# Optimization experiments

Measured on AMD Instinct MI355X. Metric: run time of the kernel, lower is better.

Reference implementation:

```python
import jax, jax.numpy as jnp
import numpy as np

B, N, C = 8, 2048, 256

def setup_inputs() -> dict:
    key = jax.random.key(0)
    ks = jax.random.split(key, 6)
    corr = jax.random.normal(ks[0], (B, N, N), dtype=jnp.float32)
    feat = jax.random.normal(ks[1], (B, N, C), dtype=jnp.float32)
    histogram = jax.random.uniform(ks[2], (B, N, 1), dtype=jnp.float32)
    mask = jax.random.normal(ks[3], (N, N), dtype=jnp.float32)
    # nn.Linear(C, C) params
    lim = 1.0 / np.sqrt(C)
    v_w = jax.random.uniform(ks[4], (C, C), minval=-lim, maxval=lim, dtype=jnp.float32)
    v_b = jax.random.uniform(ks[5], (C,), minval=-lim, maxval=lim, dtype=jnp.float32)
    return {"corr": corr, "feat": feat, "histogram": histogram, "mask": mask, "v_w": v_w, "v_b": v_b}

def reference(corr, feat, histogram, mask, v_w, v_b):
    # histogram is viewed/expanded in the original but never used downstream.
    # masked softmax over last axis: (b, n, n)
    attn = jax.nn.softmax(corr + mask[None, :, :], axis=-1)
    # v projection: y = feat @ v_w.T + v_b   (b, n, c)
    ref_feat_v = jnp.einsum("bnc,dc->bnd", feat, v_w) + v_b
    # attention output: (b, n, c)
    return jnp.einsum("bnm,bmc->bnc", attn, ref_feat_v)
```

## Files before the change

kernel.cpp:

```cpp
#include <hip/hip_runtime.h>
#include <hip/hip_fp16.h>


#define B_ 8
#define N_ 2048
#define C_ 256

typedef _Float16 half8  __attribute__((ext_vector_type(8)));
typedef _Float16 half4v __attribute__((ext_vector_type(4)));
typedef float    f32x4  __attribute__((ext_vector_type(4)));

__global__ __launch_bounds__(256) void k_convw(const float* __restrict__ w,
                                               _Float16* __restrict__ wh) {
    int i = (blockIdx.x * 256 + threadIdx.x) * 4;
    float4 v = *(const float4*)(w + i);
    half4v h = {(_Float16)v.x, (_Float16)v.y, (_Float16)v.z, (_Float16)v.w};
    *(half4v*)(wh + i) = h;
}

__global__ __launch_bounds__(256) void k_trans(const float* __restrict__ feat,
                                               _Float16* __restrict__ featF) {
    __shared__ _Float16 s[64][68];
    int blk  = blockIdx.x;
    int b    = blk >> 7;
    int tile = blk & 127;
    int n0   = (tile >> 2) << 6;
    int c0   = (tile & 3) << 6;
    int t    = threadIdx.x;

    const float* src = feat + ((size_t)(b * N_ + n0)) * C_ + c0;
#pragma unroll
    for (int i = 0; i < 4; ++i) {
        int idx = i * 256 + t;
        int row = idx >> 4;
        int c4  = (idx & 15) << 2;
        float4 v = *(const float4*)(src + (size_t)row * C_ + c4);
        half4v h = {(_Float16)v.x, (_Float16)v.y, (_Float16)v.z, (_Float16)v.w};
        *(half4v*)&s[row][c4] = h;
    }
    __syncthreads();

    int w = t >> 6, l = t & 63;
    int kk  = w & 1;
    int cb0 = (w >> 1) << 1;
#pragma unroll
    for (int cbi = 0; cbi < 2; ++cbi) {
        int cb = cb0 + cbi;
        half8 v;
#pragma unroll
        for (int j = 0; j < 8; ++j)
            v[j] = s[kk * 32 + ((l >> 4) << 3) + j][(cb << 4) + (l & 15)];
        _Float16* dst = featF +
            (((size_t)((b * 64 + (n0 >> 5) + kk) * 16 + (c0 >> 4) + cb)) * 64 + l) * 8;
        *(half8*)dst = v;
    }
}

__global__ __launch_bounds__(512, 4) void k_attn(const float* __restrict__ corr,
                                                 const float* __restrict__ mask,
                                                 const _Float16* __restrict__ featF,
                                                 _Float16* __restrict__ T) {
    __shared__ _Float16 p_lds[2][32 * 64];
    __shared__ float rowsum[32];

    const int rblk = blockIdx.x >> 3;
    const int b    = blockIdx.x & 7;
    const int r0   = rblk * 32;
    const int tg   = threadIdx.x;
    const int w    = tg >> 6, l = tg & 63;
    const int lrow = l & 15, kch = l >> 4;

    const int srow = tg >> 4;
    const int scol = (tg & 15) << 2;

    const float*    pc  = corr + ((size_t)(b * N_ + r0 + srow)) * N_ + scol;
    const float*    pm  = mask + ((size_t)(r0 + srow)) * N_ + scol;
    const _Float16* pfb = featF + ((size_t)b * (64 * 16 * 512))
                               + (((size_t)(w * 2)) * 64 + l) * 8;

    const int swaddr = srow * 64 + (((scol >> 3) ^ (srow & 7)) << 3) + (scol & 7);
    const int ag0 = ((kch ^ (lrow & 7)) << 3);
    const int ag1 = (((4 + kch) ^ (lrow & 7)) << 3);

    float rs = 0.0f;
    f32x4 acc[2][2] = {};

#define EXPSTORE(TT, CC, MM)                                                  \
    {                                                                         \
        float p0 = __expf((CC).x + (MM).x), p1 = __expf((CC).y + (MM).y);     \
        float p2 = __expf((CC).z + (MM).z), p3 = __expf((CC).w + (MM).w);     \
        rs += (p0 + p1) + (p2 + p3);                                          \
        half4v h = {(_Float16)p0, (_Float16)p1, (_Float16)p2, (_Float16)p3};  \
        *(half4v*)&p_lds[(TT) & 1][swaddr] = h;                               \
    }

    float4 cP = *(const float4*)pc;
    float4 mP = *(const float4*)pm;
    float4 cA = *(const float4*)(pc + 64);
    float4 mA = *(const float4*)(pm + 64);
    float4 cB, mB;
    EXPSTORE(0, cP, mP);
    __syncthreads();

#define STEP(T_, CCON, MCON, CLD, MLD)                                        \
    {                                                                         \
        const int t_ = (T_);                                                  \
          \
        const _Float16* pf = pfb + (size_t)t_ * 16384;                        \
        half8 b00 = *(const half8*)pf;                                        \
        half8 b01 = *(const half8*)(pf + 512);                                \
        half8 b10 = *(const half8*)(pf + 8192);                               \
        half8 b11 = *(const half8*)(pf + 8704);                               \
                                           \
        if (t_ < 30) {                                                        \
            CLD = *(const float4*)(pc + (t_ + 2) * 64);                       \
            MLD = *(const float4*)(pm + (t_ + 2) * 64);                       \
        }                                                                     \
                                                      \
        const _Float16* pl = &p_lds[t_ & 1][0];                               \
        half8 a00 = *(const half8*)&pl[lrow * 64 + ag0];                      \
        half8 a10 = *(const half8*)&pl[(16 + lrow) * 64 + ag0];               \
        half8 a01 = *(const half8*)&pl[lrow * 64 + ag1];                      \
        half8 a11 = *(const half8*)&pl[(16 + lrow) * 64 + ag1];               \
                             \
        if (t_ < 31) EXPSTORE(t_ + 1, CCON, MCON);                            \
                        \
        acc[0][0] = __builtin_amdgcn_mfma_f32_16x16x32_f16(a00, b00, acc[0][0], 0, 0, 0); \
        acc[0][1] = __builtin_amdgcn_mfma_f32_16x16x32_f16(a00, b01, acc[0][1], 0, 0, 0); \
        acc[1][0] = __builtin_amdgcn_mfma_f32_16x16x32_f16(a10, b00, acc[1][0], 0, 0, 0); \
        acc[1][1] = __builtin_amdgcn_mfma_f32_16x16x32_f16(a10, b01, acc[1][1], 0, 0, 0); \
        acc[0][0] = __builtin_amdgcn_mfma_f32_16x16x32_f16(a01, b10, acc[0][0], 0, 0, 0); \
        acc[0][1] = __builtin_amdgcn_mfma_f32_16x16x32_f16(a01, b11, acc[0][1], 0, 0, 0); \
        acc[1][0] = __builtin_amdgcn_mfma_f32_16x16x32_f16(a11, b10, acc[1][0], 0, 0, 0); \
        acc[1][1] = __builtin_amdgcn_mfma_f32_16x16x32_f16(a11, b11, acc[1][1], 0, 0, 0); \
            \
        asm volatile("s_waitcnt lgkmcnt(0)" ::: "memory");                    \
        __builtin_amdgcn_sched_barrier(0);                                    \
        __builtin_amdgcn_s_barrier();                                         \
        __builtin_amdgcn_sched_barrier(0);                                    \
    }

    for (int th = 0; th < 16; ++th) {
        STEP(2 * th,     cA, mA, cB, mB);
        STEP(2 * th + 1, cB, mB, cA, mA);
    }
#undef STEP
#undef EXPSTORE

    rs += __shfl_xor(rs, 1);
    rs += __shfl_xor(rs, 2);
    rs += __shfl_xor(rs, 4);
    rs += __shfl_xor(rs, 8);
    if ((l & 15) == 0) rowsum[srow] = rs;
    __syncthreads();

#pragma unroll
    for (int m = 0; m < 2; ++m) {
        float inv[4];
#pragma unroll
        for (int j = 0; j < 4; ++j)
            inv[j] = 1.0f / rowsum[m * 16 + kch * 4 + j];
        _Float16* pT = T + ((size_t)(b * N_ + r0 + m * 16 + kch * 4)) * C_
                         + w * 32 + lrow;
#pragma unroll
        for (int j = 0; j < 4; ++j) {
#pragma unroll
            for (int n = 0; n < 2; ++n) {
                pT[(size_t)j * C_ + n * 16] = (_Float16)(acc[m][n][j] * inv[j]);
            }
        }
    }
}

__global__ __launch_bounds__(256, 2) void k_out(const _Float16* __restrict__ T,
                                                const _Float16* __restrict__ wh,
                                                const float* __restrict__ v_b,
                                                float* __restrict__ out) {
    const int blk = blockIdx.x;
    const int r0  = blk * 32;
    const int t   = threadIdx.x;
    const int w   = t >> 6, l = t & 63;
    const int wr  = w >> 1, wc = w & 1;
    const int lrow = l & 15, kch = l >> 4;

    const _Float16* pA = T  + ((size_t)(r0 + wr * 16 + lrow)) * C_ + kch * 8;
    const _Float16* pB = wh + ((size_t)(wc * 128 + lrow)) * C_ + kch * 8;

    f32x4 acc[8] = {};
#pragma unroll
    for (int step = 0; step < 8; step++) {
        half8 a = *(const half8*)(pA + step * 32);
#pragma unroll
        for (int q = 0; q < 8; q++) {
            half8 bf = *(const half8*)(pB + step * 32 + (size_t)q * 16 * C_);
            acc[q] = __builtin_amdgcn_mfma_f32_16x16x32_f16(a, bf, acc[q], 0, 0, 0);
        }
    }

    float* pO = out + ((size_t)(r0 + wr * 16 + kch * 4)) * C_ + wc * 128 + lrow;
#pragma unroll
    for (int q = 0; q < 8; q++) {
        float bias = v_b[wc * 128 + q * 16 + lrow];
#pragma unroll
        for (int j = 0; j < 4; j++) {
            pO[(size_t)j * C_ + q * 16] = acc[q][j] + bias;
        }
    }
}

extern "C" void kernel_launch(void* const* d_in, const int* in_sizes, int n_in,
                              void* d_out, int out_size, void* d_ws, size_t ws_size,
                              hipStream_t stream) {
    const float* corr = (const float*)d_in[0];
    const float* feat = (const float*)d_in[1];
    const float* mask = (const float*)d_in[3];
    const float* v_w  = (const float*)d_in[4];
    const float* v_b  = (const float*)d_in[5];
    float* out = (float*)d_out;

    char* ws = (char*)d_ws;
    _Float16* featF = (_Float16*)ws;
    _Float16* T     = (_Float16*)(ws + (size_t)8 * 1024 * 1024);
    _Float16* wh    = (_Float16*)(ws + (size_t)16 * 1024 * 1024);

    hipLaunchKernelGGL(k_trans, dim3(1024), dim3(256), 0, stream, feat, featF);
    hipLaunchKernelGGL(k_convw, dim3(64),   dim3(256), 0, stream, v_w, wh);
    hipLaunchKernelGGL(k_attn,  dim3(512),  dim3(512), 0, stream, corr, mask, featF, T);
    hipLaunchKernelGGL(k_out,   dim3(512),  dim3(256), 0, stream, T, wh, v_b, out);
}
```

Baseline: 75.82 us.

## Retile attention kernel to 128-row by 64-column blocks with LDS-staged features

The attention kernel now gives each block 128 rows and a 64-column slice of C, laid out as a 4x2 grid of waves. Feature tiles are staged into LDS with direct global-to-LDS loads, double-buffered, so more rows reuse each feature tile. The cost is that each row's softmax exponentials and its corr/mask reads are repeated across the four column-slice blocks. Wait counts are changed so the asynchronous loads overlap with the MFMA work.

```diff
diff --git a/kernel.cpp b/kernel.cpp
--- a/kernel.cpp
+++ b/kernel.cpp
@@ -9,6 +9,13 @@
 typedef _Float16 half8  __attribute__((ext_vector_type(8)));
 typedef _Float16 half4v __attribute__((ext_vector_type(4)));
 typedef float    f32x4  __attribute__((ext_vector_type(4)));
+
+static __device__ __forceinline__ void gload_lds16(const _Float16* g, _Float16* l) {
+    __builtin_amdgcn_global_load_lds(
+        (const __attribute__((address_space(1))) unsigned int*)g,
+        (__attribute__((address_space(3))) unsigned int*)l,
+        16, 0, 0);
+}
 
 __global__ __launch_bounds__(256) void k_convw(const float* __restrict__ w,
                                                _Float16* __restrict__ wh) {
@@ -60,71 +67,105 @@
                                                  const float* __restrict__ mask,
                                                  const _Float16* __restrict__ featF,
                                                  _Float16* __restrict__ T) {
-    __shared__ _Float16 p_lds[2][32 * 64];
-    __shared__ float rowsum[32];
-
-    const int rblk = blockIdx.x >> 3;
-    const int b    = blockIdx.x & 7;
-    const int r0   = rblk * 32;
-    const int tg   = threadIdx.x;
-    const int w    = tg >> 6, l = tg & 63;
+    __shared__ _Float16 p_lds[2][128 * 64];
+    __shared__ _Float16 f_lds[2][8 * 512];
+    __shared__ float rowsum[128];
+
+    const int blk = blockIdx.x;
+    const int b   = blk & 7;
+    const int s   = blk >> 3;
+    const int rb  = s >> 2, cb = s & 3;
+    const int r0  = rb * 128;
+    const int tg  = threadIdx.x;
+    const int w   = tg >> 6, l = tg & 63;
+    const int wr  = w >> 1, wc = w & 1;
     const int lrow = l & 15, kch = l >> 4;
 
-    const int srow = tg >> 4;
-    const int scol = (tg & 15) << 2;
-
-    const float*    pc  = corr + ((size_t)(b * N_ + r0 + srow)) * N_ + scol;
-    const float*    pm  = mask + ((size_t)(r0 + srow)) * N_ + scol;
-    const _Float16* pfb = featF + ((size_t)b * (64 * 16 * 512))
-                               + (((size_t)(w * 2)) * 64 + l) * 8;
-
-    const int swaddr = srow * 64 + (((scol >> 3) ^ (srow & 7)) << 3) + (scol & 7);
+    const int srow = tg >> 2;
+    const int scol = (tg & 3) << 4;
+
+    const float* pc = corr + ((size_t)(b * N_ + r0 + srow)) * N_ + scol;
+    const float* pm = mask + ((size_t)(r0 + srow)) * N_ + scol;
+    const _Float16* pf = featF +
+        (((size_t)(b * 64 + (w >> 2)) * 16 + cb * 4 + (w & 3)) * 512) + l * 8;
+    const int fstep = 2 * 16 * 512;
+    _Float16* fd0 = &f_lds[0][w * 512 + l * 8];
+    _Float16* fd1 = &f_lds[1][w * 512 + l * 8];
+
+    int wad[4];
+#pragma unroll
+    for (int q = 0; q < 4; ++q) {
+        int col = scol + q * 4;
+        wad[q] = srow * 64 + ((((col >> 3) ^ (srow & 7)) << 3)) + (col & 7);
+    }
     const int ag0 = ((kch ^ (lrow & 7)) << 3);
     const int ag1 = (((4 + kch) ^ (lrow & 7)) << 3);
+    const int rA0 = (wr * 32 + lrow) * 64;
+    const int rA1 = (wr * 32 + 16 + lrow) * 64;
+    const int bo00 = (0 + wc * 2 + 0) * 512 + l * 8;
+    const int bo01 = (0 + wc * 2 + 1) * 512 + l * 8;
+    const int bo10 = (4 + wc * 2 + 0) * 512 + l * 8;
+    const int bo11 = (4 + wc * 2 + 1) * 512 + l * 8;
 
     float rs = 0.0f;
     f32x4 acc[2][2] = {};
 
 #define EXPSTORE(TT, CC, MM)                                                  \
     {                                                                         \
-        float p0 = __expf((CC).x + (MM).x), p1 = __expf((CC).y + (MM).y);     \
-        float p2 = __expf((CC).z + (MM).z), p3 = __expf((CC).w + (MM).w);     \
-        rs += (p0 + p1) + (p2 + p3);                                          \
-        half4v h = {(_Float16)p0, (_Float16)p1, (_Float16)p2, (_Float16)p3};  \
-        *(half4v*)&p_lds[(TT) & 1][swaddr] = h;                               \
-    }
-
-    float4 cP = *(const float4*)pc;
-    float4 mP = *(const float4*)pm;
-    float4 cA = *(const float4*)(pc + 64);
-    float4 mA = *(const float4*)(pm + 64);
-    float4 cB, mB;
-    EXPSTORE(0, cP, mP);
+        _Pragma("unroll")                                                     \
+        for (int q = 0; q < 4; ++q) {                                         \
+            float p0 = __expf((CC)[q].x + (MM)[q].x);                         \
+            float p1 = __expf((CC)[q].y + (MM)[q].y);                         \
+            float p2 = __expf((CC)[q].z + (MM)[q].z);                         \
+            float p3 = __expf((CC)[q].w + (MM)[q].w);                         \
+            rs += (p0 + p1) + (p2 + p3);                                      \
+            half4v h = {(_Float16)p0, (_Float16)p1, (_Float16)p2, (_Float16)p3}; \
+            *(half4v*)&p_lds[(TT) & 1][wad[q]] = h;                           \
+        }                                                                     \
+    }
+
+    float4 cA[4], cB[4], mM[4];
+    gload_lds16(pf, fd0);
+#pragma unroll
+    for (int q = 0; q < 4; ++q) cA[q] = *(const float4*)(pc + q * 4);
+#pragma unroll
+    for (int q = 0; q < 4; ++q) mM[q] = *(const float4*)(pm + q * 4);
+#pragma unroll
+    for (int q = 0; q < 4; ++q) cB[q] = *(const float4*)(pc + 64 + q * 4);
+    EXPSTORE(0, cA, mM);
     __syncthreads();
 
-#define STEP(T_, CCON, MCON, CLD, MLD)                                        \
+#define STEP(T_, CCON, CLD)                                                   \
     {                                                                         \
         const int t_ = (T_);                                                  \
-          \
-        const _Float16* pf = pfb + (size_t)t_ * 16384;                        \
-        half8 b00 = *(const half8*)pf;                                        \
-        half8 b01 = *(const half8*)(pf + 512);                                \
-        half8 b10 = *(const half8*)(pf + 8192);                               \
-        half8 b11 = *(const half8*)(pf + 8704);                               \
-                                           \
+           \
+        if (t_ < 31) gload_lds16(pf + (size_t)(t_ + 1) * fstep,               \
+                                 ((t_ + 1) & 1) ? fd1 : fd0);                 \
+        __builtin_amdgcn_sched_barrier(0);                                    \
+                                          \
+        if (t_ < 31) {                                                        \
+            _Pragma("unroll")                                                 \
+            for (int q = 0; q < 4; ++q)                                       \
+                mM[q] = *(const float4*)(pm + (t_ + 1) * 64 + q * 4);         \
+        }                                                                     \
+                                         \
         if (t_ < 30) {                                                        \
-            CLD = *(const float4*)(pc + (t_ + 2) * 64);                       \
-            MLD = *(const float4*)(pm + (t_ + 2) * 64);                       \
-        }                                                                     \
-                                                      \
+            _Pragma("unroll")                                                 \
+            for (int q = 0; q < 4; ++q)                                       \
+                CLD[q] = *(const float4*)(pc + (t_ + 2) * 64 + q * 4);        \
+        }                                                                     \
+                                                    \
         const _Float16* pl = &p_lds[t_ & 1][0];                               \
-        half8 a00 = *(const half8*)&pl[lrow * 64 + ag0];                      \
-        half8 a10 = *(const half8*)&pl[(16 + lrow) * 64 + ag0];               \
-        half8 a01 = *(const half8*)&pl[lrow * 64 + ag1];                      \
-        half8 a11 = *(const half8*)&pl[(16 + lrow) * 64 + ag1];               \
-                             \
-        if (t_ < 31) EXPSTORE(t_ + 1, CCON, MCON);                            \
-                        \
+        const _Float16* fb = &f_lds[t_ & 1][0];                               \
+        half8 a00 = *(const half8*)&pl[rA0 + ag0];                            \
+        half8 a10 = *(const half8*)&pl[rA1 + ag0];                            \
+        half8 a01 = *(const half8*)&pl[rA0 + ag1];                            \
+        half8 a11 = *(const half8*)&pl[rA1 + ag1];                            \
+        half8 b00 = *(const half8*)&fb[bo00];                                 \
+        half8 b01 = *(const half8*)&fb[bo01];                                 \
+        half8 b10 = *(const half8*)&fb[bo10];                                 \
+        half8 b11 = *(const half8*)&fb[bo11];                                 \
+                                                                \
         acc[0][0] = __builtin_amdgcn_mfma_f32_16x16x32_f16(a00, b00, acc[0][0], 0, 0, 0); \
         acc[0][1] = __builtin_amdgcn_mfma_f32_16x16x32_f16(a00, b01, acc[0][1], 0, 0, 0); \
         acc[1][0] = __builtin_amdgcn_mfma_f32_16x16x32_f16(a10, b00, acc[1][0], 0, 0, 0); \
@@ -133,25 +174,29 @@
         acc[0][1] = __builtin_amdgcn_mfma_f32_16x16x32_f16(a01, b11, acc[0][1], 0, 0, 0); \
         acc[1][0] = __builtin_amdgcn_mfma_f32_16x16x32_f16(a11, b10, acc[1][0], 0, 0, 0); \
         acc[1][1] = __builtin_amdgcn_mfma_f32_16x16x32_f16(a11, b11, acc[1][1], 0, 0, 0); \
-            \
-        asm volatile("s_waitcnt lgkmcnt(0)" ::: "memory");                    \
+        \
+        if (t_ < 31) EXPSTORE(t_ + 1, CCON, mM);                              \
+         \
+        if (t_ < 30) {                                                        \
+            asm volatile("s_waitcnt vmcnt(4) lgkmcnt(0)" ::: "memory");       \
+        } else {                                                              \
+            asm volatile("s_waitcnt vmcnt(0) lgkmcnt(0)" ::: "memory");       \
+        }                                                                     \
         __builtin_amdgcn_sched_barrier(0);                                    \
-        __builtin_amdgcn_s_barrier();                                         \
+        if (t_ < 31) __builtin_amdgcn_s_barrier();                            \
         __builtin_amdgcn_sched_barrier(0);                                    \
     }
 
     for (int th = 0; th < 16; ++th) {
-        STEP(2 * th,     cA, mA, cB, mB);
-        STEP(2 * th + 1, cB, mB, cA, mA);
+        STEP(2 * th,     cB, cA);
+        STEP(2 * th + 1, cA, cB);
     }
 #undef STEP
 #undef EXPSTORE
 
     rs += __shfl_xor(rs, 1);
     rs += __shfl_xor(rs, 2);
-    rs += __shfl_xor(rs, 4);
-    rs += __shfl_xor(rs, 8);
-    if ((l & 15) == 0) rowsum[srow] = rs;
+    if ((tg & 3) == 0) rowsum[srow] = rs;
     __syncthreads();
 
 #pragma unroll
@@ -159,9 +204,9 @@
         float inv[4];
 #pragma unroll
         for (int j = 0; j < 4; ++j)
-            inv[j] = 1.0f / rowsum[m * 16 + kch * 4 + j];
-        _Float16* pT = T + ((size_t)(b * N_ + r0 + m * 16 + kch * 4)) * C_
-                         + w * 32 + lrow;
+            inv[j] = 1.0f / rowsum[wr * 32 + m * 16 + kch * 4 + j];
+        _Float16* pT = T + ((size_t)(b * N_ + r0 + wr * 32 + m * 16 + kch * 4)) * C_
+                         + cb * 64 + wc * 32 + lrow;
 #pragma unroll
         for (int j = 0; j < 4; ++j) {
 #pragma unroll
```

Result: slower. 103.8 us (+37.0%).
